# Kernel tuning notes

Hardware: AMD Instinct MI355X
Metric: run time of the kernel (lower is better)

Reference implementation:

```python
import jax, jax.numpy as jnp
import numpy as np

B, L_TEXT, N_TOKEN = 8, 2048, 2048
C_TEXT, C_OUT = 3584, 384
C_HID = C_OUT * 2
CHAIN_TYPES = (1, 2)   # heavy, light
CDR_TYPES = (2, 4, 6)  # CDR1/2/3


def setup_inputs() -> dict:
    key = jax.random.key(0)
    ks = jax.random.split(key, 10)
    text_conditioning = jax.random.normal(ks[0], (B, L_TEXT, C_TEXT), jnp.float32)
    text_mask = jnp.ones((B, L_TEXT), jnp.int32)
    chain_type_ids = jax.random.randint(ks[1], (B, L_TEXT), 0, 3).astype(jnp.int32)
    cdr_region_type_ids = jax.random.randint(ks[2], (B, L_TEXT), 0, 10).astype(jnp.int32)
    boltz_chain_type = jax.random.randint(ks[3], (B, N_TOKEN), 0, 4).astype(jnp.int32)
    boltz_region_type = jax.random.randint(ks[4], (B, N_TOKEN), 0, 10).astype(jnp.int32)
    W1 = jax.random.normal(ks[5], (C_HID, C_TEXT), jnp.float32) * 0.02
    b1 = jnp.zeros((C_HID,), jnp.float32)
    W2 = jax.random.normal(ks[6], (C_OUT, C_HID), jnp.float32) * 0.02
    b2 = jnp.zeros((C_OUT,), jnp.float32)
    scale = jnp.ones((1,), jnp.float32)
    return {
        "text_conditioning": text_conditioning, "text_mask": text_mask,
        "chain_type_ids": chain_type_ids, "cdr_region_type_ids": cdr_region_type_ids,
        "boltz_chain_type": boltz_chain_type, "boltz_region_type": boltz_region_type,
        "W1": W1, "b1": b1, "W2": W2, "b2": b2, "scale": scale,
    }


def _align_one(text_proj, tmask, pmask):
    # text_proj: [L, C]; tmask: [L] bool (text CDR positions); pmask: [N] bool (protein CDR positions)
    # The k-th masked text token (in sequence order) maps to the k-th masked protein token,
    # for k < min(n_text, n_protein). Other protein positions get zeros.
    L = tmask.shape[0]
    trank = jnp.cumsum(tmask) - 1          # rank among text CDR tokens
    n_text = jnp.sum(tmask)
    prank = jnp.cumsum(pmask) - 1          # rank among protein CDR tokens
    # idx_by_rank[r] = text index whose rank is r; out-of-range scatter indices dropped
    idx_by_rank = jnp.zeros((L,), jnp.int32).at[jnp.where(tmask, trank, L)].set(
        jnp.arange(L, dtype=jnp.int32), mode="drop")
    valid = pmask & (prank < n_text)       # prank < n_protein holds by construction under pmask
    src = idx_by_rank[jnp.clip(prank, 0, L - 1)]
    emb = text_proj[src]                   # [N, C]
    return jnp.where(valid[:, None], emb, jnp.zeros((), text_proj.dtype))


def reference(text_conditioning, text_mask, chain_type_ids, cdr_region_type_ids,
              boltz_chain_type, boltz_region_type, W1, b1, W2, b2, scale):
    # 2-layer MLP projection: c_text -> 2*c_out -> c_out with SiLU
    h = jax.nn.silu(jnp.einsum("blt,ht->blh", text_conditioning, W1) + b1)
    text_proj = jnp.einsum("blh,ch->blc", h, W2) + b2    # [B, L, C_OUT]

    tm = text_mask.astype(bool)
    result = jnp.zeros((text_conditioning.shape[0], boltz_chain_type.shape[1], W2.shape[0]),
                       text_proj.dtype)
    align = jax.vmap(_align_one)
    for ct in CHAIN_TYPES:
        for rt in CDR_TYPES:
            tmask = (chain_type_ids == ct) & (cdr_region_type_ids == rt) & tm
            pmask = (boltz_chain_type == ct) & (boltz_region_type == rt)
            # (chain, cdr) pairs write to disjoint protein positions, so add is exact
            result = result + align(text_proj, tmask, pmask)
    return scale * result
```

## Files before the change

### kernel.cpp

```cpp
#include <hip/hip_runtime.h>
#include <hip/hip_bf16.h>
#include <math.h>

typedef __bf16 bf16_t;
typedef bf16_t bf16x8 __attribute__((ext_vector_type(8)));
typedef bf16_t bf16x4 __attribute__((ext_vector_type(4)));
typedef float f32x4 __attribute__((ext_vector_type(4)));

#define L_TEXT 2048
#define N_TOKEN 2048
#define C_TEXT 3584
#define C_OUT 384
#define C_HID 768
#define BATCH 8
#define MAXROWS (BATCH * N_TOKEN)
#define PM 3072
#define NPAIR (BATCH * 6)

#define NW1 (C_HID * C_TEXT / 8)
#define NW2 (C_OUT * C_HID / 8)
#define NZERO (MAXROWS * C_OUT / 4)
#define CHUNKS_TOTAL (NW1 + NW2 + NZERO)
#define CHUNK_BLOCKS (CHUNKS_TOTAL / 256)
#define GCH (C_TEXT / 8)

__global__ __launch_bounds__(256) void init_map_kernel(
    const float* __restrict__ W1, const float* __restrict__ W2,
    bf16_t* __restrict__ W1b, bf16_t* __restrict__ W2b,
    float* __restrict__ outp,
    const int* __restrict__ tm, const int* __restrict__ ctid,
    const int* __restrict__ cdrid, const int* __restrict__ bct,
    const int* __restrict__ brt,
    int* __restrict__ trowL, int* __restrict__ pidxL, int* __restrict__ vcnt) {
    if (blockIdx.x >= CHUNK_BLOCKS) {
        const int bp = blockIdx.x - CHUNK_BLOCKS;
        const int lane = threadIdx.x;
        if (lane >= 64) return;
        const int b = bp / 6, p = bp % 6;
        const int ct = (p < 3) ? 1 : 2;
        const int rt = 2 + 2 * (p % 3);
        const unsigned long long ltm = (1ull << lane) - 1ull;

        unsigned int tbits = 0, pbits = 0;
#pragma unroll
        for (int i = 0; i < 32; i++) {
            int l = i * 64 + lane;
            unsigned int m = (ctid[b * L_TEXT + l] == ct) &&
                             (cdrid[b * L_TEXT + l] == rt) &&
                             (tm[b * L_TEXT + l] != 0);
            tbits |= m << i;
        }
#pragma unroll
        for (int i = 0; i < 32; i++) {
            int n = i * 64 + lane;
            unsigned int m = (bct[b * N_TOKEN + n] == ct) &&
                             (brt[b * N_TOKEN + n] == rt);
            pbits |= m << i;
        }
        int base = 0;
#pragma unroll
        for (int i = 0; i < 32; i++) {
            bool m = (tbits >> i) & 1;
            unsigned long long bal = __ballot(m);
            if (m) trowL[bp * L_TEXT + base + __popcll(bal & ltm)] = i * 64 + lane;
            base += __popcll(bal);
        }
        const int n_text = base;
        base = 0;
#pragma unroll
        for (int i = 0; i < 32; i++) {
            bool m = (pbits >> i) & 1;
            unsigned long long bal = __ballot(m);
            if (m) pidxL[bp * L_TEXT + base + __popcll(bal & ltm)] = i * 64 + lane;
            base += __popcll(bal);
        }
        const int n_prot = base;
        if (lane == 0) vcnt[bp] = n_text < n_prot ? n_text : n_prot;
        return;
    }
    int idx = blockIdx.x * 256 + threadIdx.x;
    if (idx < NW1) {
        int i = idx * 8;
        float4 v0 = *(const float4*)(W1 + i);
        float4 v1 = *(const float4*)(W1 + i + 4);
        bf16x8 o;
        o[0] = (bf16_t)v0.x; o[1] = (bf16_t)v0.y; o[2] = (bf16_t)v0.z; o[3] = (bf16_t)v0.w;
        o[4] = (bf16_t)v1.x; o[5] = (bf16_t)v1.y; o[6] = (bf16_t)v1.z; o[7] = (bf16_t)v1.w;
        *(bf16x8*)(W1b + i) = o;
    } else if (idx < NW1 + NW2) {
        int i = (idx - NW1) * 8;
        float4 v0 = *(const float4*)(W2 + i);
        float4 v1 = *(const float4*)(W2 + i + 4);
        bf16x8 o;
        o[0] = (bf16_t)v0.x; o[1] = (bf16_t)v0.y; o[2] = (bf16_t)v0.z; o[3] = (bf16_t)v0.w;
        o[4] = (bf16_t)v1.x; o[5] = (bf16_t)v1.y; o[6] = (bf16_t)v1.z; o[7] = (bf16_t)v1.w;
        *(bf16x8*)(W2b + i) = o;
    } else {
        int z = idx - NW1 - NW2;
        f32x4 zv = (f32x4){0.f, 0.f, 0.f, 0.f};
        *(f32x4*)(outp + (size_t)z * 4) = zv;
    }
}

__global__ __launch_bounds__(64) void map_write_kernel(
    const int* __restrict__ trowL, const int* __restrict__ pidxL,
    const int* __restrict__ vcnt,
    int* __restrict__ rows_src, int* __restrict__ rows_dst,
    int* __restrict__ count) {
    const int bp = blockIdx.x;
    const int b = bp / 6;
    const int lane = threadIdx.x;
    int base = 0, total = 0;
    for (int q = 0; q < NPAIR; q++) {
        int v = vcnt[q];
        if (q < bp) base += v;
        total += v;
    }
    if (bp == 0 && lane == 0) *count = total < PM ? total : PM;
    const int v = vcnt[bp];
    for (int r = lane; r < v; r += 64) {
        int g = base + r;
        if (g < PM) {
            rows_src[g] = b * L_TEXT + trowL[bp * L_TEXT + r];
            rows_dst[g] = b * N_TOKEN + pidxL[bp * L_TEXT + r];
        }
    }
}

__global__ __launch_bounds__(256) void gather_kernel(
    const float* __restrict__ X, const int* __restrict__ rows_src,
    const int* __restrict__ countp, bf16_t* __restrict__ Xg) {
    int count = *countp; if (count > PM) count = PM;
    int idx = blockIdx.x * 256 + threadIdx.x;
    int m = idx / GCH;
    if (m >= count) return;
    int c = (idx % GCH) * 8;
    const float* src = X + (size_t)rows_src[m] * C_TEXT + c;
    float4 v0 = *(const float4*)(src);
    float4 v1 = *(const float4*)(src + 4);
    bf16x8 o;
    o[0] = (bf16_t)v0.x; o[1] = (bf16_t)v0.y; o[2] = (bf16_t)v0.z; o[3] = (bf16_t)v0.w;
    o[4] = (bf16_t)v1.x; o[5] = (bf16_t)v1.y; o[6] = (bf16_t)v1.z; o[7] = (bf16_t)v1.w;
    *(bf16x8*)(Xg + (size_t)m * C_TEXT + c) = o;
}

__global__ __launch_bounds__(256) void gemm1_kernel(
    const bf16_t* __restrict__ Xg, const bf16_t* __restrict__ W1b,
    const float* __restrict__ b1, const int* __restrict__ countp,
    bf16_t* __restrict__ H) {
    int count = *countp; if (count > PM) count = PM;
    const int m0 = blockIdx.x * 64;
    if (m0 >= count) return;
    const int n0 = blockIdx.y * 128;

    __shared__ __align__(16) bf16_t As[2][64][40];
    __shared__ __align__(16) bf16_t Bs[2][128][40];

    const int t = threadIdx.x;
    const int lane = t & 63;
    const int w = t >> 6;
    const int wr = w >> 1, wc = w & 1;
    const int fr = lane & 15;
    const int kq = (lane >> 4) * 8;

    f32x4 acc[2][4];
#pragma unroll
    for (int i = 0; i < 2; i++)
#pragma unroll
        for (int j = 0; j < 4; j++) acc[i][j] = (f32x4){0.f, 0.f, 0.f, 0.f};

    const int arow = t >> 2, ac8 = (t & 3) * 8;
    const bf16_t* ap = Xg + (size_t)(m0 + arow) * C_TEXT + ac8;
    const int aofs = arow * 40 + ac8;
    const bf16_t* bp[2];
    int bofs[2];
#pragma unroll
    for (int j = 0; j < 2; j++) {
        int c = t + 256 * j;
        int row = c >> 2, c8 = (c & 3) * 8;
        bp[j] = W1b + (size_t)(n0 + row) * C_TEXT + c8;
        bofs[j] = row * 40 + c8;
    }

    bf16_t* AsF = &As[0][0][0];
    bf16_t* BsF = &Bs[0][0][0];
    const int ABUF = 64 * 40, BBUF = 128 * 40;

    bf16x8 ra = *(const bf16x8*)(ap);
    bf16x8 rb0 = *(const bf16x8*)(bp[0]);
    bf16x8 rb1 = *(const bf16x8*)(bp[1]);

    const int T = C_TEXT / 32;
    for (int tile = 0; tile < T; ++tile) {
        const int cur = tile & 1;
        *(bf16x8*)(AsF + cur * ABUF + aofs) = ra;
        *(bf16x8*)(BsF + cur * BBUF + bofs[0]) = rb0;
        *(bf16x8*)(BsF + cur * BBUF + bofs[1]) = rb1;
        bf16x8 na, nb0, nb1;
        bool more = (tile + 1 < T);
        if (more) {
            int k = (tile + 1) * 32;
            na = *(const bf16x8*)(ap + k);
            nb0 = *(const bf16x8*)(bp[0] + k);
            nb1 = *(const bf16x8*)(bp[1] + k);
        }
        __syncthreads();
        bf16x8 af[2], bfr[4];
#pragma unroll
        for (int mi = 0; mi < 2; mi++)
            af[mi] = *(const bf16x8*)(AsF + cur * ABUF + (wr * 32 + mi * 16 + fr) * 40 + kq);
#pragma unroll
        for (int ni = 0; ni < 4; ni++)
            bfr[ni] = *(const bf16x8*)(BsF + cur * BBUF + (wc * 64 + ni * 16 + fr) * 40 + kq);
#pragma unroll
        for (int mi = 0; mi < 2; mi++)
#pragma unroll
            for (int ni = 0; ni < 4; ni++)
                acc[mi][ni] = __builtin_amdgcn_mfma_f32_16x16x32_bf16(
                    af[mi], bfr[ni], acc[mi][ni], 0, 0, 0);
        if (more) { ra = na; rb0 = nb0; rb1 = nb1; }
        __syncthreads();
    }

    const int rj = (lane >> 4) * 4;
#pragma unroll
    for (int mi = 0; mi < 2; mi++) {
#pragma unroll
        for (int ni = 0; ni < 4; ni++) {
            int gn = n0 + wc * 64 + ni * 16 + fr;
            float bias = b1[gn];
#pragma unroll
            for (int j = 0; j < 4; j++) {
                int gm = m0 + wr * 32 + mi * 16 + rj + j;
                if (gm < count) {
                    float v = acc[mi][ni][j] + bias;
                    H[(size_t)gm * C_HID + gn] = (bf16_t)(v / (1.0f + __expf(-v)));
                }
            }
        }
    }
}

__global__ __launch_bounds__(256) void gemm2_kernel(
    const bf16_t* __restrict__ Hm, const bf16_t* __restrict__ W2b,
    const float* __restrict__ b2, const int* __restrict__ rows_dst,
    const int* __restrict__ countp, const float* __restrict__ scale,
    float* __restrict__ outp) {
    int count = *countp; if (count > PM) count = PM;
    const int m0 = blockIdx.x * 32;
    if (m0 >= count) return;
    const int n0 = blockIdx.y * 128;

    __shared__ __align__(16) bf16_t As[2][32][40];
    __shared__ __align__(16) bf16_t Bs[2][128][40];

    const int t = threadIdx.x;
    const int lane = t & 63;
    const int w = t >> 6;
    const int fr = lane & 15;
    const int kq = (lane >> 4) * 8;

    f32x4 acc[2][2];
#pragma unroll
    for (int i = 0; i < 2; i++)
#pragma unroll
        for (int j = 0; j < 2; j++) acc[i][j] = (f32x4){0.f, 0.f, 0.f, 0.f};

    const int arow = t >> 2, ac8 = (t & 3) * 8;
    const bool astage = (t < 128);
    const bf16_t* ap = Hm + (size_t)(m0 + arow) * C_HID + ac8;
    const int aofs = arow * 40 + ac8;
    const bf16_t* bp[2];
    int bofs[2];
#pragma unroll
    for (int j = 0; j < 2; j++) {
        int c = t + 256 * j;
        int row = c >> 2, c8 = (c & 3) * 8;
        bp[j] = W2b + (size_t)(n0 + row) * C_HID + c8;
        bofs[j] = row * 40 + c8;
    }

    bf16_t* AsF = &As[0][0][0];
    bf16_t* BsF = &Bs[0][0][0];
    const int ABUF = 32 * 40, BBUF = 128 * 40;

    bf16x8 ra;
    if (astage) ra = *(const bf16x8*)(ap);
    bf16x8 rb0 = *(const bf16x8*)(bp[0]);
    bf16x8 rb1 = *(const bf16x8*)(bp[1]);

    const int T = C_HID / 32;
    for (int tile = 0; tile < T; ++tile) {
        const int cur = tile & 1;
        if (astage) *(bf16x8*)(AsF + cur * ABUF + aofs) = ra;
        *(bf16x8*)(BsF + cur * BBUF + bofs[0]) = rb0;
        *(bf16x8*)(BsF + cur * BBUF + bofs[1]) = rb1;
        bf16x8 na, nb0, nb1;
        bool more = (tile + 1 < T);
        if (more) {
            int k = (tile + 1) * 32;
            if (astage) na = *(const bf16x8*)(ap + k);
            nb0 = *(const bf16x8*)(bp[0] + k);
            nb1 = *(const bf16x8*)(bp[1] + k);
        }
        __syncthreads();
        bf16x8 af[2], bfr[2];
#pragma unroll
        for (int mi = 0; mi < 2; mi++)
            af[mi] = *(const bf16x8*)(AsF + cur * ABUF + (mi * 16 + fr) * 40 + kq);
#pragma unroll
        for (int ni = 0; ni < 2; ni++)
            bfr[ni] = *(const bf16x8*)(BsF + cur * BBUF + (w * 32 + ni * 16 + fr) * 40 + kq);
#pragma unroll
        for (int mi = 0; mi < 2; mi++)
#pragma unroll
            for (int ni = 0; ni < 2; ni++)
                acc[mi][ni] = __builtin_amdgcn_mfma_f32_16x16x32_bf16(
                    af[mi], bfr[ni], acc[mi][ni], 0, 0, 0);
        if (more) { if (astage) ra = na; rb0 = nb0; rb1 = nb1; }
        __syncthreads();
    }

    const float sc = scale[0];
    const int rj = (lane >> 4) * 4;
#pragma unroll
    for (int mi = 0; mi < 2; mi++) {
#pragma unroll
        for (int ni = 0; ni < 2; ni++) {
            int gn = n0 + w * 32 + ni * 16 + fr;
            float bias = b2[gn];
#pragma unroll
            for (int j = 0; j < 2 * 2; j++) ;
#pragma unroll
            for (int j = 0; j < 4; j++) {
                int gm = m0 + mi * 16 + rj + j;
                if (gm < count) {
                    int dst = rows_dst[gm];
                    outp[(size_t)dst * C_OUT + gn] = sc * (acc[mi][ni][j] + bias);
                }
            }
        }
    }
}

extern "C" void kernel_launch(void* const* d_in, const int* in_sizes, int n_in,
                              void* d_out, int out_size, void* d_ws, size_t ws_size,
                              hipStream_t stream) {
    const float* X     = (const float*)d_in[0];
    const int*   tm    = (const int*)d_in[1];
    const int*   ctid  = (const int*)d_in[2];
    const int*   cdrid = (const int*)d_in[3];
    const int*   bct   = (const int*)d_in[4];
    const int*   brt   = (const int*)d_in[5];
    const float* W1    = (const float*)d_in[6];
    const float* b1    = (const float*)d_in[7];
    const float* W2    = (const float*)d_in[8];
    const float* b2    = (const float*)d_in[9];
    const float* scale = (const float*)d_in[10];

    char* ws = (char*)d_ws;
    size_t off = 0;
    int* count = (int*)(ws + off);        off += 1024;
    int* vcnt = (int*)(ws + off);         off += 1024;
    int* rows_src = (int*)(ws + off);     off += (size_t)PM * 4;
    int* rows_dst = (int*)(ws + off);     off += (size_t)PM * 4;
    int* trowL = (int*)(ws + off);        off += (size_t)NPAIR * L_TEXT * 4;
    int* pidxL = (int*)(ws + off);        off += (size_t)NPAIR * L_TEXT * 4;
    bf16_t* W1b = (bf16_t*)(ws + off);    off += (size_t)C_HID * C_TEXT * 2;
    bf16_t* W2b = (bf16_t*)(ws + off);    off += (size_t)C_OUT * C_HID * 2;
    bf16_t* Xg = (bf16_t*)(ws + off);     off += (size_t)PM * C_TEXT * 2;
    bf16_t* H = (bf16_t*)(ws + off);      off += (size_t)PM * C_HID * 2;
    float* outp = (float*)d_out;

    init_map_kernel<<<CHUNK_BLOCKS + NPAIR, 256, 0, stream>>>(
        W1, W2, W1b, W2b, outp, tm, ctid, cdrid, bct, brt, trowL, pidxL, vcnt);

    map_write_kernel<<<NPAIR, 64, 0, stream>>>(trowL, pidxL, vcnt,
                                               rows_src, rows_dst, count);

    gather_kernel<<<(PM * GCH) / 256, 256, 0, stream>>>(X, rows_src, count, Xg);

    dim3 g1(PM / 64, C_HID / 128);
    gemm1_kernel<<<g1, 256, 0, stream>>>(Xg, W1b, b1, count, H);

    dim3 g2(PM / 32, C_OUT / 128);
    gemm2_kernel<<<g2, 256, 0, stream>>>(H, W2b, b2, rows_dst, count, scale, outp);
}
```

Before: 142.8 us.

## Split-K the first GEMM with 128x128 tiles and a separate bias+SiLU reduce

The first projection GEMM now splits its 3584-long K dimension four ways across a third grid axis and uses larger 128x128 tiles. Each split writes fp32 partial sums to a workspace buffer, and a new reduce kernel adds them, applies the bias and SiLU, and writes bf16 H. The goal is more blocks in flight and a shorter serial K loop per block on a GPU that was under-filled by roughly 230 active tiles. The trailing per-tile barrier is removed, which stays safe with double buffering. In exchange it adds an extra kernel launch and several MB of fp32 partial-sum writes and reads.

```diff
diff --git a/kernel.cpp b/kernel.cpp
--- a/kernel.cpp
+++ b/kernel.cpp
@@ -16,6 +16,8 @@
 #define MAXROWS (BATCH * N_TOKEN)
 #define PM 3072
 #define NPAIR (BATCH * 6)
+#define KSPLIT 4
+#define KCHUNK (C_TEXT / KSPLIT)
 
 #define NW1 (C_HID * C_TEXT / 8)
 #define NW2 (C_OUT * C_HID / 8)
@@ -146,14 +148,14 @@
 
 __global__ __launch_bounds__(256) void gemm1_kernel(
     const bf16_t* __restrict__ Xg, const bf16_t* __restrict__ W1b,
-    const float* __restrict__ b1, const int* __restrict__ countp,
-    bf16_t* __restrict__ H) {
+    const int* __restrict__ countp, float* __restrict__ P) {
     int count = *countp; if (count > PM) count = PM;
-    const int m0 = blockIdx.x * 64;
+    const int m0 = blockIdx.x * 128;
     if (m0 >= count) return;
     const int n0 = blockIdx.y * 128;
-
-    __shared__ __align__(16) bf16_t As[2][64][40];
+    const int kbeg = blockIdx.z * KCHUNK;
+
+    __shared__ __align__(16) bf16_t As[2][128][40];
     __shared__ __align__(16) bf16_t Bs[2][128][40];
 
     const int t = threadIdx.x;
@@ -163,82 +165,106 @@
     const int fr = lane & 15;
     const int kq = (lane >> 4) * 8;
 
-    f32x4 acc[2][4];
-#pragma unroll
-    for (int i = 0; i < 2; i++)
+    f32x4 acc[4][4];
+#pragma unroll
+    for (int i = 0; i < 4; i++)
 #pragma unroll
         for (int j = 0; j < 4; j++) acc[i][j] = (f32x4){0.f, 0.f, 0.f, 0.f};
 
-    const int arow = t >> 2, ac8 = (t & 3) * 8;
-    const bf16_t* ap = Xg + (size_t)(m0 + arow) * C_TEXT + ac8;
-    const int aofs = arow * 40 + ac8;
+    const bf16_t* ap[2];
     const bf16_t* bp[2];
-    int bofs[2];
+    int ofs[2];
 #pragma unroll
     for (int j = 0; j < 2; j++) {
         int c = t + 256 * j;
         int row = c >> 2, c8 = (c & 3) * 8;
-        bp[j] = W1b + (size_t)(n0 + row) * C_TEXT + c8;
-        bofs[j] = row * 40 + c8;
+        ap[j] = Xg + (size_t)(m0 + row) * C_TEXT + kbeg + c8;
+        bp[j] = W1b + (size_t)(n0 + row) * C_TEXT + kbeg + c8;
+        ofs[j] = row * 40 + c8;
     }
 
     bf16_t* AsF = &As[0][0][0];
     bf16_t* BsF = &Bs[0][0][0];
-    const int ABUF = 64 * 40, BBUF = 128 * 40;
-
-    bf16x8 ra = *(const bf16x8*)(ap);
-    bf16x8 rb0 = *(const bf16x8*)(bp[0]);
-    bf16x8 rb1 = *(const bf16x8*)(bp[1]);
-
-    const int T = C_TEXT / 32;
+    const int BUF = 128 * 40;
+
+    bf16x8 ra[2], rb[2];
+#pragma unroll
+    for (int j = 0; j < 2; j++) { ra[j] = *(const bf16x8*)(ap[j]); rb[j] = *(const bf16x8*)(bp[j]); }
+
+    const int T = KCHUNK / 32;
     for (int tile = 0; tile < T; ++tile) {
         const int cur = tile & 1;
-        *(bf16x8*)(AsF + cur * ABUF + aofs) = ra;
-        *(bf16x8*)(BsF + cur * BBUF + bofs[0]) = rb0;
-        *(bf16x8*)(BsF + cur * BBUF + bofs[1]) = rb1;
-        bf16x8 na, nb0, nb1;
+#pragma unroll
+        for (int j = 0; j < 2; j++) {
+            *(bf16x8*)(AsF + cur * BUF + ofs[j]) = ra[j];
+            *(bf16x8*)(BsF + cur * BUF + ofs[j]) = rb[j];
+        }
+        bf16x8 na[2], nb[2];
         bool more = (tile + 1 < T);
         if (more) {
             int k = (tile + 1) * 32;
-            na = *(const bf16x8*)(ap + k);
-            nb0 = *(const bf16x8*)(bp[0] + k);
-            nb1 = *(const bf16x8*)(bp[1] + k);
+#pragma unroll
+            for (int j = 0; j < 2; j++) {
+                na[j] = *(const bf16x8*)(ap[j] + k);
+                nb[j] = *(const bf16x8*)(bp[j] + k);
+            }
         }
         __syncthreads();
-        bf16x8 af[2], bfr[4];
-#pragma unroll
-        for (int mi = 0; mi < 2; mi++)
-            af[mi] = *(const bf16x8*)(AsF + cur * ABUF + (wr * 32 + mi * 16 + fr) * 40 + kq);
+        bf16x8 af[4], bfr[4];
+#pragma unroll
+        for (int mi = 0; mi < 4; mi++)
+            af[mi] = *(const bf16x8*)(AsF + cur * BUF + (wr * 64 + mi * 16 + fr) * 40 + kq);
 #pragma unroll
         for (int ni = 0; ni < 4; ni++)
-            bfr[ni] = *(const bf16x8*)(BsF + cur * BBUF + (wc * 64 + ni * 16 + fr) * 40 + kq);
-#pragma unroll
-        for (int mi = 0; mi < 2; mi++)
+            bfr[ni] = *(const bf16x8*)(BsF + cur * BUF + (wc * 64 + ni * 16 + fr) * 40 + kq);
+#pragma unroll
+        for (int mi = 0; mi < 4; mi++)
 #pragma unroll
             for (int ni = 0; ni < 4; ni++)
                 acc[mi][ni] = __builtin_amdgcn_mfma_f32_16x16x32_bf16(
                     af[mi], bfr[ni], acc[mi][ni], 0, 0, 0);
-        if (more) { ra = na; rb0 = nb0; rb1 = nb1; }
-        __syncthreads();
-    }
-
+        if (more) {
+#pragma unroll
+            for (int j = 0; j < 2; j++) { ra[j] = na[j]; rb[j] = nb[j]; }
+        }
+    }
+
+    float* Pk = P + (size_t)blockIdx.z * PM * C_HID;
     const int rj = (lane >> 4) * 4;
 #pragma unroll
-    for (int mi = 0; mi < 2; mi++) {
+    for (int mi = 0; mi < 4; mi++) {
 #pragma unroll
         for (int ni = 0; ni < 4; ni++) {
             int gn = n0 + wc * 64 + ni * 16 + fr;
-            float bias = b1[gn];
 #pragma unroll
             for (int j = 0; j < 4; j++) {
-                int gm = m0 + wr * 32 + mi * 16 + rj + j;
-                if (gm < count) {
-                    float v = acc[mi][ni][j] + bias;
-                    H[(size_t)gm * C_HID + gn] = (bf16_t)(v / (1.0f + __expf(-v)));
-                }
+                int gm = m0 + wr * 64 + mi * 16 + rj + j;
+                if (gm < count) Pk[(size_t)gm * C_HID + gn] = acc[mi][ni][j];
             }
         }
     }
+}
+
+__global__ __launch_bounds__(256) void reduce1_kernel(
+    const float* __restrict__ P, const float* __restrict__ b1,
+    const int* __restrict__ countp, bf16_t* __restrict__ H) {
+    int count = *countp; if (count > PM) count = PM;
+    int idx = blockIdx.x * 256 + threadIdx.x;
+    int m = idx / (C_HID / 4);
+    int c = (idx % (C_HID / 4)) * 4;
+    if (m >= count) return;
+    f32x4 s = *(const f32x4*)(P + (size_t)m * C_HID + c);
+#pragma unroll
+    for (int ks = 1; ks < KSPLIT; ks++)
+        s += *(const f32x4*)(P + ((size_t)ks * PM + m) * C_HID + c);
+    f32x4 bb = *(const f32x4*)(b1 + c);
+    bf16x4 o;
+#pragma unroll
+    for (int j = 0; j < 4; j++) {
+        float v = s[j] + bb[j];
+        o[j] = (bf16_t)(v / (1.0f + __expf(-v)));
+    }
+    *(bf16x4*)(H + (size_t)m * C_HID + c) = o;
 }
 
 __global__ __launch_bounds__(256) void gemm2_kernel(
@@ -329,8 +355,6 @@
         for (int ni = 0; ni < 2; ni++) {
             int gn = n0 + w * 32 + ni * 16 + fr;
             float bias = b2[gn];
-#pragma unroll
-            for (int j = 0; j < 2 * 2; j++) ;
 #pragma unroll
             for (int j = 0; j < 4; j++) {
                 int gm = m0 + mi * 16 + rj + j;
@@ -370,6 +394,7 @@
     bf16_t* W2b = (bf16_t*)(ws + off);    off += (size_t)C_OUT * C_HID * 2;
     bf16_t* Xg = (bf16_t*)(ws + off);     off += (size_t)PM * C_TEXT * 2;
     bf16_t* H = (bf16_t*)(ws + off);      off += (size_t)PM * C_HID * 2;
+    float* P = (float*)(ws + off);        off += (size_t)KSPLIT * PM * C_HID * 4;
     float* outp = (float*)d_out;
 
     init_map_kernel<<<CHUNK_BLOCKS + NPAIR, 256, 0, stream>>>(
@@ -380,8 +405,10 @@
 
     gather_kernel<<<(PM * GCH) / 256, 256, 0, stream>>>(X, rows_src, count, Xg);
 
-    dim3 g1(PM / 64, C_HID / 128);
-    gemm1_kernel<<<g1, 256, 0, stream>>>(Xg, W1b, b1, count, H);
+    dim3 g1(PM / 128, C_HID / 128, KSPLIT);
+    gemm1_kernel<<<g1, 256, 0, stream>>>(Xg, W1b, count, P);
+
+    reduce1_kernel<<<(PM * C_HID / 4) / 256, 256, 0, stream>>>(P, b1, count, H);
 
     dim3 g2(PM / 32, C_OUT / 128);
     gemm2_kernel<<<g2, 256, 0, stream>>>(H, W2b, b2, rows_dst, count, scale, outp);
```

New measurement: 124.8 us. -12.7%, faster.

## Split-K the first GEMM four ways with a separate reduce+bias+SiLU kernel

Applied to the files above, without the earlier changes.

The first projection GEMM now splits the 3584-long K dimension into four chunks along a third grid axis. Each chunk writes fp32 partial sums to a workspace buffer, and a new reduce kernel sums them, adds the bias, applies SiLU and writes bf16 H. The goal is more blocks, so the GPU fills up when only a few thousand gathered rows exist. The cost is extra fp32 partial traffic and one more kernel launch. The redundant trailing __syncthreads in the double-buffered k-loop is also removed.

```diff
diff --git a/kernel.cpp b/kernel.cpp
--- a/kernel.cpp
+++ b/kernel.cpp
@@ -16,6 +16,8 @@
 #define MAXROWS (BATCH * N_TOKEN)
 #define PM 3072
 #define NPAIR (BATCH * 6)
+#define KSPLIT 4
+#define KCHUNK (C_TEXT / KSPLIT)
 
 #define NW1 (C_HID * C_TEXT / 8)
 #define NW2 (C_OUT * C_HID / 8)
@@ -146,12 +148,12 @@
 
 __global__ __launch_bounds__(256) void gemm1_kernel(
     const bf16_t* __restrict__ Xg, const bf16_t* __restrict__ W1b,
-    const float* __restrict__ b1, const int* __restrict__ countp,
-    bf16_t* __restrict__ H) {
+    const int* __restrict__ countp, float* __restrict__ P) {
     int count = *countp; if (count > PM) count = PM;
     const int m0 = blockIdx.x * 64;
     if (m0 >= count) return;
     const int n0 = blockIdx.y * 128;
+    const int kbeg = blockIdx.z * KCHUNK;
 
     __shared__ __align__(16) bf16_t As[2][64][40];
     __shared__ __align__(16) bf16_t Bs[2][128][40];
@@ -170,7 +172,7 @@
         for (int j = 0; j < 4; j++) acc[i][j] = (f32x4){0.f, 0.f, 0.f, 0.f};
 
     const int arow = t >> 2, ac8 = (t & 3) * 8;
-    const bf16_t* ap = Xg + (size_t)(m0 + arow) * C_TEXT + ac8;
+    const bf16_t* ap = Xg + (size_t)(m0 + arow) * C_TEXT + kbeg + ac8;
     const int aofs = arow * 40 + ac8;
     const bf16_t* bp[2];
     int bofs[2];
@@ -178,7 +180,7 @@
     for (int j = 0; j < 2; j++) {
         int c = t + 256 * j;
         int row = c >> 2, c8 = (c & 3) * 8;
-        bp[j] = W1b + (size_t)(n0 + row) * C_TEXT + c8;
+        bp[j] = W1b + (size_t)(n0 + row) * C_TEXT + kbeg + c8;
         bofs[j] = row * 40 + c8;
     }
 
@@ -190,7 +192,7 @@
     bf16x8 rb0 = *(const bf16x8*)(bp[0]);
     bf16x8 rb1 = *(const bf16x8*)(bp[1]);
 
-    const int T = C_TEXT / 32;
+    const int T = KCHUNK / 32;
     for (int tile = 0; tile < T; ++tile) {
         const int cur = tile & 1;
         *(bf16x8*)(AsF + cur * ABUF + aofs) = ra;
@@ -219,26 +221,44 @@
                 acc[mi][ni] = __builtin_amdgcn_mfma_f32_16x16x32_bf16(
                     af[mi], bfr[ni], acc[mi][ni], 0, 0, 0);
         if (more) { ra = na; rb0 = nb0; rb1 = nb1; }
-        __syncthreads();
-    }
-
+    }
+
+    float* Pk = P + (size_t)blockIdx.z * PM * C_HID;
     const int rj = (lane >> 4) * 4;
 #pragma unroll
     for (int mi = 0; mi < 2; mi++) {
 #pragma unroll
         for (int ni = 0; ni < 4; ni++) {
             int gn = n0 + wc * 64 + ni * 16 + fr;
-            float bias = b1[gn];
 #pragma unroll
             for (int j = 0; j < 4; j++) {
                 int gm = m0 + wr * 32 + mi * 16 + rj + j;
-                if (gm < count) {
-                    float v = acc[mi][ni][j] + bias;
-                    H[(size_t)gm * C_HID + gn] = (bf16_t)(v / (1.0f + __expf(-v)));
-                }
+                if (gm < count) Pk[(size_t)gm * C_HID + gn] = acc[mi][ni][j];
             }
         }
     }
+}
+
+__global__ __launch_bounds__(256) void reduce1_kernel(
+    const float* __restrict__ P, const float* __restrict__ b1,
+    const int* __restrict__ countp, bf16_t* __restrict__ H) {
+    int count = *countp; if (count > PM) count = PM;
+    int idx = blockIdx.x * 256 + threadIdx.x;
+    int m = idx / (C_HID / 4);
+    int c = (idx % (C_HID / 4)) * 4;
+    if (m >= count) return;
+    f32x4 s = *(const f32x4*)(P + (size_t)m * C_HID + c);
+#pragma unroll
+    for (int ks = 1; ks < KSPLIT; ks++)
+        s += *(const f32x4*)(P + ((size_t)ks * PM + m) * C_HID + c);
+    f32x4 bb = *(const f32x4*)(b1 + c);
+    bf16x4 o;
+#pragma unroll
+    for (int j = 0; j < 4; j++) {
+        float v = s[j] + bb[j];
+        o[j] = (bf16_t)(v / (1.0f + __expf(-v)));
+    }
+    *(bf16x4*)(H + (size_t)m * C_HID + c) = o;
 }
 
 __global__ __launch_bounds__(256) void gemm2_kernel(
@@ -329,8 +349,6 @@
         for (int ni = 0; ni < 2; ni++) {
             int gn = n0 + w * 32 + ni * 16 + fr;
             float bias = b2[gn];
-#pragma unroll
-            for (int j = 0; j < 2 * 2; j++) ;
 #pragma unroll
             for (int j = 0; j < 4; j++) {
                 int gm = m0 + mi * 16 + rj + j;
@@ -370,6 +388,7 @@
     bf16_t* W2b = (bf16_t*)(ws + off);    off += (size_t)C_OUT * C_HID * 2;
     bf16_t* Xg = (bf16_t*)(ws + off);     off += (size_t)PM * C_TEXT * 2;
     bf16_t* H = (bf16_t*)(ws + off);      off += (size_t)PM * C_HID * 2;
+    float* P = (float*)(ws + off);        off += (size_t)KSPLIT * PM * C_HID * 4;
     float* outp = (float*)d_out;
 
     init_map_kernel<<<CHUNK_BLOCKS + NPAIR, 256, 0, stream>>>(
@@ -380,8 +399,10 @@
 
     gather_kernel<<<(PM * GCH) / 256, 256, 0, stream>>>(X, rows_src, count, Xg);
 
-    dim3 g1(PM / 64, C_HID / 128);
-    gemm1_kernel<<<g1, 256, 0, stream>>>(Xg, W1b, b1, count, H);
+    dim3 g1(PM / 64, C_HID / 128, KSPLIT);
+    gemm1_kernel<<<g1, 256, 0, stream>>>(Xg, W1b, count, P);
+
+    reduce1_kernel<<<(PM * C_HID / 4) / 256, 256, 0, stream>>>(P, b1, count, H);
 
     dim3 g2(PM / 32, C_OUT / 128);
     gemm2_kernel<<<g2, 256, 0, stream>>>(H, W2b, b2, rows_dst, count, scale, outp);
```

New measurement: 124.9 us. -12.5%, faster.
